# Kernel tuning notes

Measured on AMD Instinct MI355X. Metric: run time of the kernel, lower is better.

The kernel has to match this reference:

```python
import jax, jax.numpy as jnp
import numpy as np

B, C, H, W = 4, 128, 64, 64
CQ = C // 8  # query/key channels = 16


def setup_inputs() -> dict:
    key = jax.random.key(0)
    ks = jax.random.split(key, 8)
    s = 0.05
    return {
        "x": jax.random.normal(ks[0], (B, C, H, W), jnp.float32),
        "wq": jax.random.normal(ks[1], (CQ, C), jnp.float32) * s,
        "bq": jax.random.normal(ks[2], (CQ,), jnp.float32) * s,
        "wk": jax.random.normal(ks[3], (CQ, C), jnp.float32) * s,
        "bk": jax.random.normal(ks[4], (CQ,), jnp.float32) * s,
        "wv": jax.random.normal(ks[5], (C, C), jnp.float32) * s,
        "bv": jax.random.normal(ks[6], (C,), jnp.float32) * s,
        # original inits gamma to 0; use small nonzero so attention path is exercised
        "gamma": jax.random.normal(ks[7], (1,), jnp.float32) * 0.1,
    }


def reference(x, wq, bq, wk, bk, wv, bv, gamma):
    b, c, h, w = x.shape
    n = h * w
    xf = x.reshape(b, c, n)  # [B, C, N]
    # 1x1 convs are per-position linear maps over channels
    q = jnp.einsum("qc,bcn->bnq", wq, xf) + bq            # [B, N, Cq]
    k = jnp.einsum("qc,bcn->bqn", wk, xf) + bk[:, None]   # [B, Cq, N]
    v = jnp.einsum("oc,bcn->bon", wv, xf) + bv[:, None]   # [B, C, N]
    # unscaled scores, softmax over keys (last dim), as in the original
    attn = jax.nn.softmax(jnp.einsum("bnq,bqm->bnm", q, k), axis=-1)  # [B, N, N]
    # out = value @ attention^T : out[b,c,n] = sum_m v[b,c,m] * attn[b,n,m]
    out = jnp.einsum("bom,bnm->bon", v, attn)             # [B, C, N]
    return gamma[0] * out.reshape(b, c, h, w) + x
```

## Files before the change

kernel.cpp:

```cpp
#include <hip/hip_runtime.h>
#include <hip/hip_bf16.h>

typedef float f32x4  __attribute__((ext_vector_type(4)));
typedef float f32x16 __attribute__((ext_vector_type(16)));
typedef short s16x8  __attribute__((ext_vector_type(8)));

#define NB 4
#define NC 128
#define NNPOS 4096
#define KSP 8
#define LOG2E 1.44269504088896f

__device__ __forceinline__ short bf16s(float x) {
    __hip_bfloat16 h = __float2bfloat16(x);
    return *reinterpret_cast<short*>(&h);
}
__device__ __forceinline__ int packbf2(float lo, float hi) {
    __hip_bfloat162 t = __float22bfloat162_rn(float2{lo, hi});
    return *reinterpret_cast<int*>(&t);
}
__device__ __forceinline__ float bf2f(unsigned short u) {
    unsigned int v = ((unsigned int)u) << 16;
    return *reinterpret_cast<float*>(&v);
}
__device__ __forceinline__ float exp2fast(float x) {
    return __builtin_amdgcn_exp2f(x);
}

__global__ __launch_bounds__(256) void qkv_kernel(
    const float* __restrict__ x,
    const float* __restrict__ wq, const float* __restrict__ bq,
    const float* __restrict__ wk, const float* __restrict__ bk,
    const float* __restrict__ wv, const float* __restrict__ bv,
    short* __restrict__ qb, short* __restrict__ kb, short* __restrict__ vt)
{
    const int n0  = blockIdx.x * 32;
    const int b   = blockIdx.y;
    const int tid = threadIdx.x;
    const int w = tid >> 6, lane = tid & 63, quad = lane >> 4, nn = lane & 15;

    __shared__ __align__(16) short xsT[32 * 136];

    #pragma unroll
    for (int p = 0; p < 4; ++p) {
        int idx = tid + p * 256;
        int cc = idx >> 3, n4 = (idx & 7) * 4;
        f32x4 xv = *(const f32x4*)&x[((size_t)(b * NC + cc)) * NNPOS + n0 + n4];
        #pragma unroll
        for (int j = 0; j < 4; ++j)
            xsT[(n4 + j) * 136 + cc] = bf16s(xv[j]);
    }

    s16x8 af[3][4];
    bool  live[3];
    f32x4 biasv[3];
    #pragma unroll
    for (int t = 0; t < 3; ++t) {
        int rid = 3 * w + t;
        int R   = rid * 16;
        const float* wsrc = nullptr; const float* bsrc = nullptr; int row0 = 0;
        float scale = 1.0f;
        if (rid < 8)        { wsrc = wv; bsrc = bv; row0 = R; }
        else if (rid == 8)  { wsrc = wq; bsrc = bq; row0 = 0; scale = LOG2E; }
        else if (rid == 10) { wsrc = wk; bsrc = bk; row0 = 0; }
        live[t] = (wsrc != nullptr);
        #pragma unroll
        for (int r = 0; r < 4; ++r)
            biasv[t][r] = live[t] ? scale * bsrc[row0 + quad * 4 + r] : 0.0f;
        if (live[t]) {
            #pragma unroll
            for (int ks = 0; ks < 4; ++ks) {
                const float* src = wsrc + (size_t)(row0 + nn) * NC + ks * 32 + quad * 8;
                f32x4 wa = *(const f32x4*)src;
                f32x4 wb = *(const f32x4*)(src + 4);
                s16x8 f;
                #pragma unroll
                for (int j = 0; j < 4; ++j) {
                    f[j]     = bf16s(scale * wa[j]);
                    f[j + 4] = bf16s(scale * wb[j]);
                }
                af[t][ks] = f;
            }
        }
    }
    __syncthreads();

    f32x4 acc[3][2];
    #pragma unroll
    for (int t = 0; t < 3; ++t)
        #pragma unroll
        for (int nt = 0; nt < 2; ++nt)
            acc[t][nt] = biasv[t];

    #pragma unroll
    for (int nt = 0; nt < 2; ++nt) {
        s16x8 bf[4];
        #pragma unroll
        for (int ks = 0; ks < 4; ++ks)
            bf[ks] = *(const s16x8*)&xsT[(nt * 16 + nn) * 136 + ks * 32 + quad * 8];
        #pragma unroll
        for (int t = 0; t < 3; ++t)
            if (live[t])
                #pragma unroll
                for (int ks = 0; ks < 4; ++ks)
                    acc[t][nt] = __builtin_amdgcn_mfma_f32_16x16x32_bf16(af[t][ks], bf[ks], acc[t][nt], 0, 0, 0);
    }

    const int slot = (nn & 3) | ((nn & 4) << 1) | ((nn & 8) >> 1);

    #pragma unroll
    for (int t = 0; t < 3; ++t) {
        if (!live[t]) continue;
        int R = (3 * w + t) * 16;
        #pragma unroll
        for (int nt = 0; nt < 2; ++nt) {
            int n = n0 + nt * 16 + nn;
            int kg = (n0 + nt * 16) >> 4;
            #pragma unroll
            for (int r = 0; r < 4; ++r) {
                short v = bf16s(acc[t][nt][r]);
                int row = R + quad * 4 + r;
                if (row < 128) {
                    int ct = row >> 5, c31r = row & 31;
                    vt[((((size_t)b * 256 + kg) * 4 + ct) * 32 + c31r) * 16 + slot] = v;
                } else if (row < 144)
                    qb[((size_t)(b * NNPOS) + n) * 16 + (row - 128)] = v;
                else
                    kb[((size_t)(b * NNPOS) + n) * 16 + (row - 160)] = v;
            }
        }
    }
}

__global__ __launch_bounds__(256, 4) void attn_kernel(
    const short* __restrict__ qb, const short* __restrict__ kb,
    const short* __restrict__ vt,
    unsigned short* __restrict__ Ow, float* __restrict__ lw)
{
    const int s   = blockIdx.x;
    const int b   = blockIdx.z;
    const int tid = threadIdx.x;
    const int w = tid >> 6, lane = tid & 63, h = lane >> 5, c31 = lane & 31;
    const int chalf = w & 1;
    const int q0 = (blockIdx.y * 2 + (w >> 1)) * 32;

    s16x8 bq = *(const s16x8*)(qb + ((size_t)(b * NNPOS) + q0 + c31) * 16 + h * 8);

    f32x16 acc[2];
    #pragma unroll
    for (int ctl = 0; ctl < 2; ++ctl)
        #pragma unroll
        for (int r = 0; r < 16; ++r) acc[ctl][r] = 0.0f;
    float lp0 = 0.f, lp1 = 0.f;

    const short* kbp = kb + (size_t)(b * NNPOS) * 16;
    const short* vbp = vt + (size_t)b * (256 * 4 * 512);
    const int mbase = s * (NNPOS / KSP);
    const int kgbase = mbase >> 4;
    const int voff = (c31 << 4) + (h << 3);
    const int NIT = (NNPOS / KSP) / 64;

    for (int it = 0; it < NIT; ++it) {
        const int m0 = mbase + it * 64;
        const int kg0 = kgbase + it * 4;

        s16x8 ak0 = *(const s16x8*)(kbp + (size_t)(m0      + c31) * 16 + h * 8);
        s16x8 ak1 = *(const s16x8*)(kbp + (size_t)(m0 + 32 + c31) * 16 + h * 8);
        s16x8 vb[4][2];
        #pragma unroll
        for (int p = 0; p < 4; ++p)
            #pragma unroll
            for (int ctl = 0; ctl < 2; ++ctl)
                vb[p][ctl] = *(const s16x8*)(vbp +
                    (((size_t)(kg0 + p) * 4 + (chalf * 2 + ctl)) << 9) + voff);

        f32x16 z;
        #pragma unroll
        for (int r = 0; r < 16; ++r) z[r] = 0.0f;
        f32x16 s0 = __builtin_amdgcn_mfma_f32_32x32x16_bf16(ak0, bq, z, 0, 0, 0);
        f32x16 s1 = __builtin_amdgcn_mfma_f32_32x32x16_bf16(ak1, bq, z, 0, 0, 0);

        s16x8 pa[4];
        #pragma unroll
        for (int p = 0; p < 4; ++p) {
            const f32x16& sv = (p < 2) ? s0 : s1;
            const int off = (p & 1) * 8;
            union { int i[4]; s16x8 v; } u;
            #pragma unroll
            for (int j = 0; j < 4; ++j) {
                float p0 = exp2fast(sv[off + 2 * j]);
                float p1 = exp2fast(sv[off + 2 * j + 1]);
                if (j & 1) lp1 += p0 + p1; else lp0 += p0 + p1;
                u.i[j] = packbf2(p0, p1);
            }
            pa[p] = u.v;
        }

        #pragma unroll
        for (int p = 0; p < 4; ++p)
            #pragma unroll
            for (int ctl = 0; ctl < 2; ++ctl)
                acc[ctl] = __builtin_amdgcn_mfma_f32_32x32x16_bf16(
                    pa[p], vb[p][ctl], acc[ctl], 0, 0, 0);
    }

    float lp = lp0 + lp1;
    lp += __shfl_xor(lp, 32, 64);
    if (chalf == 0 && lane < 32)
        lw[((size_t)(b * KSP + s)) * NNPOS + q0 + c31] = lp;

    #pragma unroll
    for (int ctl = 0; ctl < 2; ++ctl) {
        const int c = (chalf * 2 + ctl) * 32 + c31;
        #pragma unroll
        for (int r = 0; r < 16; ++r) {
            int q = q0 + (r & 3) + 8 * (r >> 2) + 4 * h;
            Ow[(((size_t)(b * KSP + s)) * NNPOS + q) * NC + c] =
                (unsigned short)bf16s(acc[ctl][r]);
        }
    }
}

__global__ __launch_bounds__(256) void combine_kernel(
    const unsigned short* __restrict__ Ow, const float* __restrict__ lw,
    const float* __restrict__ x, const float* __restrict__ gamma,
    float* __restrict__ out)
{
    const int n0  = blockIdx.x * 64;
    const int b   = blockIdx.y;
    const int tid = threadIdx.x;

    __shared__ float ot[128 * 65 + 64];
    float* lsum = ot + 128 * 65;

    if (tid < 64) {
        float sl = 0.f;
        #pragma unroll
        for (int sI = 0; sI < KSP; ++sI)
            sl += lw[((size_t)(b * KSP + sI)) * NNPOS + n0 + tid];
        lsum[tid] = sl;
    }
    __syncthreads();

    #pragma unroll
    for (int p = 0; p < 8; ++p) {
        int e = tid + p * 256;
        int cq = e & 31, n = e >> 5;
        float a0 = 0.f, a1 = 0.f, a2 = 0.f, a3 = 0.f;
        #pragma unroll
        for (int sI = 0; sI < KSP; ++sI) {
            const unsigned short* src = Ow +
                (((size_t)(b * KSP + sI)) * NNPOS + n0 + n) * NC + cq * 4;
            ushort4 u = *(const ushort4*)src;
            a0 += bf2f(u.x); a1 += bf2f(u.y); a2 += bf2f(u.z); a3 += bf2f(u.w);
        }
        float inv = 1.0f / lsum[n];
        ot[(cq * 4) * 65 + n]     = a0 * inv;
        ot[(cq * 4 + 1) * 65 + n] = a1 * inv;
        ot[(cq * 4 + 2) * 65 + n] = a2 * inv;
        ot[(cq * 4 + 3) * 65 + n] = a3 * inv;
    }
    __syncthreads();

    const float g = gamma[0];
    #pragma unroll
    for (int p = 0; p < 32; ++p) {
        int e = tid + p * 256;
        int n = e & 63, c = e >> 6;
        size_t a = ((size_t)(b * NC + c)) * NNPOS + n0 + n;
        out[a] = g * ot[c * 65 + n] + x[a];
    }
}

extern "C" void kernel_launch(void* const* d_in, const int* in_sizes, int n_in,
                              void* d_out, int out_size, void* d_ws, size_t ws_size,
                              hipStream_t stream) {
    const float* x     = (const float*)d_in[0];
    const float* wq    = (const float*)d_in[1];
    const float* bq    = (const float*)d_in[2];
    const float* wk    = (const float*)d_in[3];
    const float* bk    = (const float*)d_in[4];
    const float* wv    = (const float*)d_in[5];
    const float* bv    = (const float*)d_in[6];
    const float* gamma = (const float*)d_in[7];
    float* out = (float*)d_out;

    short* qb = (short*)d_ws;
    short* kb = qb + (size_t)NB * NNPOS * 16;
    short* vt = kb + (size_t)NB * NNPOS * 16;
    unsigned short* Ow = (unsigned short*)(vt + (size_t)NB * NC * NNPOS);
    float* lw = (float*)(Ow + (size_t)NB * KSP * NNPOS * NC);

    qkv_kernel<<<dim3(128, NB), 256, 0, stream>>>(x, wq, bq, wk, bk, wv, bv, qb, kb, vt);
    attn_kernel<<<dim3(KSP, 64, NB), 256, 0, stream>>>(qb, kb, vt, Ow, lw);
    combine_kernel<<<dim3(NNPOS / 64, NB), 256, 0, stream>>>(Ow, lw, x, gamma, out);
}
```

Before: 123.7 us.

## Stage V tiles in double-buffered LDS shared across 8 waves per block

```diff
diff --git a/kernel.cpp b/kernel.cpp
--- a/kernel.cpp
+++ b/kernel.cpp
@@ -132,7 +132,7 @@
     }
 }
 
-__global__ __launch_bounds__(256, 4) void attn_kernel(
+__global__ __launch_bounds__(512, 4) void attn_kernel(
     const short* __restrict__ qb, const short* __restrict__ kb,
     const short* __restrict__ vt,
     unsigned short* __restrict__ Ow, float* __restrict__ lw)
@@ -142,7 +142,9 @@
     const int tid = threadIdx.x;
     const int w = tid >> 6, lane = tid & 63, h = lane >> 5, c31 = lane & 31;
     const int chalf = w & 1;
-    const int q0 = (blockIdx.y * 2 + (w >> 1)) * 32;
+    const int q0 = blockIdx.y * 128 + (w >> 1) * 32;
+
+    __shared__ __align__(16) short vts[2][8192];
 
     s16x8 bq = *(const s16x8*)(qb + ((size_t)(b * NNPOS) + q0 + c31) * 16 + h * 8);
 
@@ -154,33 +156,63 @@
     float lp0 = 0.f, lp1 = 0.f;
 
     const short* kbp = kb + (size_t)(b * NNPOS) * 16;
-    const short* vbp = vt + (size_t)b * (256 * 4 * 512);
+    const short* vcb = vt + (size_t)b * (256 * 4 * 512);
     const int mbase = s * (NNPOS / KSP);
     const int kgbase = mbase >> 4;
-    const int voff = (c31 << 4) + (h << 3);
     const int NIT = (NNPOS / KSP) / 64;
+    const int cp0 = tid * 8, cp1 = (tid + 512) * 8;
+
+    {
+        const short* src = vcb + (size_t)kgbase * 2048;
+        uint4 a = *(const uint4*)(src + cp0);
+        uint4 c = *(const uint4*)(src + cp1);
+        *(uint4*)(&vts[0][cp0]) = a;
+        *(uint4*)(&vts[0][cp1]) = c;
+    }
+    s16x8 akb[2][2];
+    #pragma unroll
+    for (int kt = 0; kt < 2; ++kt)
+        akb[0][kt] = *(const s16x8*)(kbp + (size_t)(mbase + kt * 32 + c31) * 16 + h * 8);
 
     for (int it = 0; it < NIT; ++it) {
-        const int m0 = mbase + it * 64;
-        const int kg0 = kgbase + it * 4;
-
-        s16x8 ak0 = *(const s16x8*)(kbp + (size_t)(m0      + c31) * 16 + h * 8);
-        s16x8 ak1 = *(const s16x8*)(kbp + (size_t)(m0 + 32 + c31) * 16 + h * 8);
-        s16x8 vb[4][2];
-        #pragma unroll
-        for (int p = 0; p < 4; ++p)
+        const int cur = it & 1, nxt = cur ^ 1;
+
+        __syncthreads();
+
+        uint4 pf0, pf1;
+        const bool haveNext = (it + 1 < NIT);
+        if (haveNext) {
+            const short* src = vcb + (size_t)(kgbase + (it + 1) * 4) * 2048;
+            pf0 = *(const uint4*)(src + cp0);
+            pf1 = *(const uint4*)(src + cp1);
+            const int m1 = mbase + (it + 1) * 64;
+            #pragma unroll
+            for (int kt = 0; kt < 2; ++kt)
+                akb[nxt][kt] = *(const s16x8*)(kbp + (size_t)(m1 + kt * 32 + c31) * 16 + h * 8);
+        }
+
+        s16x8 vb01[2][2];
+        #pragma unroll
+        for (int p = 0; p < 2; ++p)
             #pragma unroll
             for (int ctl = 0; ctl < 2; ++ctl)
-                vb[p][ctl] = *(const s16x8*)(vbp +
-                    (((size_t)(kg0 + p) * 4 + (chalf * 2 + ctl)) << 9) + voff);
+                vb01[p][ctl] = *(const s16x8*)(&vts[cur][
+                    (p * 4 + chalf * 2 + ctl) * 512 + c31 * 16 + h * 8]);
 
         f32x16 z;
         #pragma unroll
         for (int r = 0; r < 16; ++r) z[r] = 0.0f;
-        f32x16 s0 = __builtin_amdgcn_mfma_f32_32x32x16_bf16(ak0, bq, z, 0, 0, 0);
-        f32x16 s1 = __builtin_amdgcn_mfma_f32_32x32x16_bf16(ak1, bq, z, 0, 0, 0);
-
-        s16x8 pa[4];
+        f32x16 s0 = __builtin_amdgcn_mfma_f32_32x32x16_bf16(akb[cur][0], bq, z, 0, 0, 0);
+        f32x16 s1 = __builtin_amdgcn_mfma_f32_32x32x16_bf16(akb[cur][1], bq, z, 0, 0, 0);
+
+        s16x8 vb23[2][2];
+        #pragma unroll
+        for (int p = 0; p < 2; ++p)
+            #pragma unroll
+            for (int ctl = 0; ctl < 2; ++ctl)
+                vb23[p][ctl] = *(const s16x8*)(&vts[cur][
+                    ((2 + p) * 4 + chalf * 2 + ctl) * 512 + c31 * 16 + h * 8]);
+
         #pragma unroll
         for (int p = 0; p < 4; ++p) {
             const f32x16& sv = (p < 2) ? s0 : s1;
@@ -188,20 +220,22 @@
             union { int i[4]; s16x8 v; } u;
             #pragma unroll
             for (int j = 0; j < 4; ++j) {
-                float p0 = exp2fast(sv[off + 2 * j]);
-                float p1 = exp2fast(sv[off + 2 * j + 1]);
-                if (j & 1) lp1 += p0 + p1; else lp0 += p0 + p1;
-                u.i[j] = packbf2(p0, p1);
+                float e0 = exp2fast(sv[off + 2 * j]);
+                float e1 = exp2fast(sv[off + 2 * j + 1]);
+                if (j & 1) lp1 += e0 + e1; else lp0 += e0 + e1;
+                u.i[j] = packbf2(e0, e1);
             }
-            pa[p] = u.v;
-        }
-
-        #pragma unroll
-        for (int p = 0; p < 4; ++p)
+            const s16x8* vbp2 = (p < 2) ? vb01[p] : vb23[p - 2];
             #pragma unroll
             for (int ctl = 0; ctl < 2; ++ctl)
                 acc[ctl] = __builtin_amdgcn_mfma_f32_32x32x16_bf16(
-                    pa[p], vb[p][ctl], acc[ctl], 0, 0, 0);
+                    u.v, vbp2[ctl], acc[ctl], 0, 0, 0);
+        }
+
+        if (haveNext) {
+            *(uint4*)(&vts[nxt][cp0]) = pf0;
+            *(uint4*)(&vts[nxt][cp1]) = pf1;
+        }
     }
 
     float lp = lp0 + lp1;
@@ -292,6 +326,6 @@
     float* lw = (float*)(Ow + (size_t)NB * KSP * NNPOS * NC);
 
     qkv_kernel<<<dim3(128, NB), 256, 0, stream>>>(x, wq, bq, wk, bk, wv, bv, qb, kb, vt);
-    attn_kernel<<<dim3(KSP, 64, NB), 256, 0, stream>>>(qb, kb, vt, Ow, lw);
+    attn_kernel<<<dim3(KSP, 32, NB), 512, 0, stream>>>(qb, kb, vt, Ow, lw);
     combine_kernel<<<dim3(NNPOS / 64, NB), 256, 0, stream>>>(Ow, lw, x, gamma, out);
 }
```

After: 128.6 us. 1.04x slower.
